# Performance work log

Hardware: AMD Instinct MI355X
Metric: run time of the kernel (lower is better)

Reference implementation:

```python
import jax, jax.numpy as jnp
import numpy as np

B, T, I, D = 16, 128, 8, 128


def layer_norm(x, g, b, eps=1e-5):
    mu = jnp.mean(x, -1, keepdims=True)
    var = jnp.mean((x - mu) ** 2, -1, keepdims=True)
    return (x - mu) * jax.lax.rsqrt(var + eps) * g + b


def setup_inputs() -> dict:
    key = jax.random.key(0)
    ks = jax.random.split(key, 8)
    vectors = jax.random.normal(ks[0], (B, T, T, I), jnp.float32)
    # structured pairwise mask: mask[b,i,j] = real[b,i] & real[b,j]
    lengths = jax.random.randint(ks[1], (B,), T // 2, T + 1)
    real = jnp.arange(T)[None, :] < lengths[:, None]  # [B,T]
    mask = real[:, :, None] & real[:, None, :]  # [B,T,T]
    s = lambda n: 1.0 / np.sqrt(n)
    W_embed = jax.random.normal(ks[2], (I, D), jnp.float32) * s(I)
    b_embed = jnp.zeros((D,), jnp.float32)
    ln1_g = jnp.ones((D,), jnp.float32)
    ln1_b = jnp.zeros((D,), jnp.float32)
    Wq = jax.random.normal(ks[3], (D, D), jnp.float32) * s(D)
    Wk = jax.random.normal(ks[4], (D, D), jnp.float32) * s(D)
    Wv = jax.random.normal(ks[5], (D, D), jnp.float32) * s(D)
    W_out = jax.random.normal(ks[6], (D, D), jnp.float32) * s(D)
    b_out = jnp.zeros((D,), jnp.float32)
    ln2_g = jnp.ones((D,), jnp.float32)
    ln2_b = jnp.zeros((D,), jnp.float32)
    return dict(vectors=vectors, mask=mask, W_embed=W_embed, b_embed=b_embed,
                ln1_g=ln1_g, ln1_b=ln1_b, Wq=Wq, Wk=Wk, Wv=Wv,
                W_out=W_out, b_out=b_out, ln2_g=ln2_g, ln2_b=ln2_b)


def reference(vectors, mask, W_embed, b_embed, ln1_g, ln1_b, Wq, Wk, Wv,
              W_out, b_out, ln2_g, ln2_b):
    Bs, Tn = vectors.shape[0], vectors.shape[1]
    Dm = W_embed.shape[1]
    square_mask = jnp.transpose(mask, (1, 2, 0))            # [T,T,B] bool
    seq = square_mask[jnp.arange(Tn), jnp.arange(Tn)]       # [T,B] bool (diagonal)
    # shared embedding stack (masked) + norm, on flattened [T*T,B,*]
    x = jnp.transpose(vectors.reshape(Bs, Tn * Tn, -1), (1, 0, 2))  # [T*T,B,I]
    mflat = square_mask.reshape(Tn * Tn, Bs, 1).astype(x.dtype)
    x = jax.nn.gelu(x @ W_embed + b_embed) * mflat
    x = layer_norm(x, ln1_g, ln1_b)
    x = x.reshape(Tn, Tn, Bs, Dm)                           # [T,T,B,D]
    keys = x @ Wk                                            # [T,T,B,D]
    values = x @ Wv                                          # [T,T,B,D]
    queries = x[jnp.arange(Tn), jnp.arange(Tn)] @ Wq         # diag gather -> [T,B,D]
    # attention mask: pairwise-real OR self
    amask = square_mask | jnp.eye(Tn, dtype=bool)[:, :, None]  # [T,T,B]
    logits = jnp.einsum('rbd,rcbd->rcb', queries, keys) / np.sqrt(Dm)
    logits = logits + jnp.where(amask, 0.0, -1e9)
    w = jax.nn.softmax(logits, axis=1)                       # [T,T,B]
    emb = jnp.einsum('rcb,rcbd->rbd', w, values)             # [T,B,D]
    # output linear block with skip connection, masked by sequence mask
    seq_f = seq[:, :, None].astype(emb.dtype)                # [T,B,1]
    h = jax.nn.gelu(emb @ W_out + b_out)
    embeddings = layer_norm(h + emb, ln2_g, ln2_b) * seq_f   # [T,B,D]
    padding_mask = ~jnp.transpose(seq)                       # [B,T]
    sequence_mask = seq[:, :, None]                          # [T,B,1]
    global_mask = jnp.ones((Tn,), dtype=bool)                # [T]
    return embeddings, padding_mask, sequence_mask, global_mask
```

## Files before the change

kernel.cpp:

```cpp
#include <hip/hip_runtime.h>
#include <hip/hip_fp16.h>
#include <math.h>

#define BB 16
#define TT 128
#define II 8
#define DD 128
#define SCALE 0.08838834764831845f

#define WS_LEN_OFF 16384


__device__ __forceinline__ float sgelu(float x) {
    float x2 = x * x;
    float w = x * (-1.5957691216f - 0.07135481627f * x2);
    float e = __expf(w);
    return __fdividef(x, 1.0f + e);
}

__device__ __forceinline__ float fast_gelu(float x) {
    float u = 1.5957691216057308f * x * (1.0f + 0.044715f * x * x);
    float e = __expf(u);
    float th = 1.0f - __fdividef(2.0f, e + 1.0f);
    return 0.5f * x * (1.0f + th);
}

__global__ void k0_compute_M(const float* __restrict__ Wq,
                             const float* __restrict__ Wk,
                             const int* __restrict__ mask,
                             float* __restrict__ M,
                             int* __restrict__ lens) {
    if (blockIdx.x == DD) {
        __shared__ int cnt[BB];
        int t = threadIdx.x;
        if (t < BB) cnt[t] = 0;
        __syncthreads();
        if (t < TT) {
            for (int b = 0; b < BB; b++) {
                if (mask[b * TT * TT + t * TT + t]) atomicAdd(&cnt[b], 1);
            }
        }
        __syncthreads();
        if (t < BB) lens[t] = cnt[t];
        return;
    }
    __shared__ float wq[DD];
    int a = blockIdx.x, e = threadIdx.x;
    wq[e] = Wq[a * DD + e];
    __syncthreads();
    const float4* wk4 = (const float4*)(Wk + e * DD);
    float acc = 0.0f;
    #pragma unroll 8
    for (int d4 = 0; d4 < DD / 4; d4++) {
        float4 w = wk4[d4];
        acc += wq[d4 * 4 + 0] * w.x + wq[d4 * 4 + 1] * w.y +
               wq[d4 * 4 + 2] * w.z + wq[d4 * 4 + 3] * w.w;
    }
    M[a * DD + e] = acc;
}

__global__ __launch_bounds__(256, 4)
void k_main(const float* __restrict__ vectors,
            const int* __restrict__ lens,
            const float* __restrict__ We,
            const float* __restrict__ be,
            const float* __restrict__ g1,
            const float* __restrict__ b1,
            const float* __restrict__ M,
            const float* __restrict__ Wv,
            const float* __restrict__ Wo,
            const float* __restrict__ bo,
            const float* __restrict__ g2,
            const float* __restrict__ b2,
            float* __restrict__ out) {
    __shared__ __half2 xsh[TT * 64];
    __shared__ float  xrs[DD];
    __shared__ float  kqs[DD];
    __shared__ float  lgt[TT];
    __shared__ float  wgt[TT];
    __shared__ float2 pbuf[256];
    __shared__ float2 sv2[64];
    __shared__ float2 emb2[64];

    int n = blockIdx.x;
    int b = n >> 7, r = n & 127;
    int t = threadIdx.x, wave = t >> 6, lane = t & 63;
    int hh = lane >> 5, sl = lane & 31;
    int dl = sl * 4;
    int len = lens[b];

    if (r >= len) {
        if (wave == 0) {
            int rb_out = r * BB + b;
            ((float2*)out)[rb_out * 64 + lane] = make_float2(0.0f, 0.0f);
            if (lane == 0) {
                out[262144 + b * TT + r] = 1.0f;
                out[264192 + r * BB + b] = 0.0f;
                if (b == 0) out[266240 + r] = 1.0f;
            }
        }
        return;
    }

    const float4* vb4 = (const float4*)(vectors + (size_t)n * TT * II);

    float4 we4[II];
    #pragma unroll
    for (int i = 0; i < II; i++) we4[i] = *(const float4*)(We + i * DD + dl);
    float4 be4 = *(const float4*)(be + dl);
    float4 g14 = *(const float4*)(g1 + dl);
    float4 b14 = *(const float4*)(b1 + dl);

    {
        float4 v0 = vb4[2 * r], v1 = vb4[2 * r + 1];
        float vv[8] = {v0.x, v0.y, v0.z, v0.w, v1.x, v1.y, v1.z, v1.w};
        float e0 = be4.x, e1 = be4.y, e2 = be4.z, e3 = be4.w;
        #pragma unroll
        for (int i = 0; i < II; i++) {
            e0 += vv[i] * we4[i].x; e1 += vv[i] * we4[i].y;
            e2 += vv[i] * we4[i].z; e3 += vv[i] * we4[i].w;
        }
        float a0 = sgelu(e0), a1 = sgelu(e1), a2 = sgelu(e2), a3 = sgelu(e3);
        float s = (a0 + a1) + (a2 + a3);
        float q = (a0 * a0 + a1 * a1) + (a2 * a2 + a3 * a3);
        #pragma unroll
        for (int o = 16; o >= 1; o >>= 1) {
            s += __shfl_xor(s, o, 64); q += __shfl_xor(q, o, 64);
        }
        float mu = s * (1.0f / 128.0f);
        float rstd = rsqrtf(q * (1.0f / 128.0f) - mu * mu + 1e-5f);
        float x0 = (a0 - mu) * rstd * g14.x + b14.x;
        float x1 = (a1 - mu) * rstd * g14.y + b14.y;
        float x2 = (a2 - mu) * rstd * g14.z + b14.z;
        float x3 = (a3 - mu) * rstd * g14.w + b14.w;
        if (t < 32) ((float4*)xrs)[sl] = make_float4(x0, x1, x2, x3);
    }
    __syncthreads();

    {
        const float2* M2 = (const float2*)M;
        float ax = 0.0f, ay = 0.0f;
        #pragma unroll 8
        for (int j = 0; j < 32; j++) {
            int a = (wave << 5) + j;
            float xv = xrs[a];
            float2 m2 = M2[a * 64 + lane];
            ax += xv * m2.x; ay += xv * m2.y;
        }
        pbuf[t] = make_float2(ax, ay);
    }
    __syncthreads();
    if (t < 64) {
        float2 p0 = pbuf[t], p1 = pbuf[64 + t], p2 = pbuf[128 + t], p3 = pbuf[192 + t];
        kqs[2 * t]     = (p0.x + p1.x + p2.x + p3.x) * SCALE;
        kqs[2 * t + 1] = (p0.y + p1.y + p2.y + p3.y) * SCALE;
    }
    __syncthreads();

    float4 kq4 = *(const float4*)&kqs[dl];
    float4 u4 = make_float4(g14.x * kq4.x, g14.y * kq4.y, g14.z * kq4.z, g14.w * kq4.w);
    float Us, C0;
    {
        float us = (u4.x + u4.y) + (u4.z + u4.w);
        float c0 = (b14.x * kq4.x + b14.y * kq4.y) + (b14.z * kq4.z + b14.w * kq4.w);
        #pragma unroll
        for (int o = 16; o >= 1; o >>= 1) {
            us += __shfl_xor(us, o, 64); c0 += __shfl_xor(c0, o, 64);
        }
        Us = us; C0 = c0;
    }

    {
        int g = (wave << 1) + hh;
        int jmax = (len - g + 15) >> 4;
        for (int j = 0; j < jmax; j++) {
            int cA = (j << 4) + g;
            int cB = cA + 8;
            float4 vA0 = vb4[2 * cA], vA1 = vb4[2 * cA + 1];
            float4 vB0 = vb4[2 * cB], vB1 = vb4[2 * cB + 1];
            float vA[8] = {vA0.x, vA0.y, vA0.z, vA0.w, vA1.x, vA1.y, vA1.z, vA1.w};
            float vB[8] = {vB0.x, vB0.y, vB0.z, vB0.w, vB1.x, vB1.y, vB1.z, vB1.w};
            float eA0 = be4.x, eA1 = be4.y, eA2 = be4.z, eA3 = be4.w;
            float eB0 = be4.x, eB1 = be4.y, eB2 = be4.z, eB3 = be4.w;
            #pragma unroll
            for (int i = 0; i < II; i++) {
                eA0 += vA[i] * we4[i].x; eA1 += vA[i] * we4[i].y;
                eA2 += vA[i] * we4[i].z; eA3 += vA[i] * we4[i].w;
                eB0 += vB[i] * we4[i].x; eB1 += vB[i] * we4[i].y;
                eB2 += vB[i] * we4[i].z; eB3 += vB[i] * we4[i].w;
            }
            float aA0 = sgelu(eA0), aA1 = sgelu(eA1), aA2 = sgelu(eA2), aA3 = sgelu(eA3);
            float aB0 = sgelu(eB0), aB1 = sgelu(eB1), aB2 = sgelu(eB2), aB3 = sgelu(eB3);
            float sA = (aA0 + aA1) + (aA2 + aA3);
            float qA = (aA0 * aA0 + aA1 * aA1) + (aA2 * aA2 + aA3 * aA3);
            float pA = (aA0 * u4.x + aA1 * u4.y) + (aA2 * u4.z + aA3 * u4.w);
            float sB = (aB0 + aB1) + (aB2 + aB3);
            float qB = (aB0 * aB0 + aB1 * aB1) + (aB2 * aB2 + aB3 * aB3);
            float pB = (aB0 * u4.x + aB1 * u4.y) + (aB2 * u4.z + aB3 * u4.w);
            #pragma unroll
            for (int o = 16; o >= 1; o >>= 1) {
                sA += __shfl_xor(sA, o, 64); qA += __shfl_xor(qA, o, 64);
                pA += __shfl_xor(pA, o, 64);
                sB += __shfl_xor(sB, o, 64); qB += __shfl_xor(qB, o, 64);
                pB += __shfl_xor(pB, o, 64);
            }
            float muA = sA * (1.0f / 128.0f), muB = sB * (1.0f / 128.0f);
            float rsA = rsqrtf(qA * (1.0f / 128.0f) - muA * muA + 1e-5f);
            float rsB = rsqrtf(qB * (1.0f / 128.0f) - muB * muB + 1e-5f);
            float xA0 = (aA0 - muA) * rsA * g14.x + b14.x;
            float xA1 = (aA1 - muA) * rsA * g14.y + b14.y;
            float xA2 = (aA2 - muA) * rsA * g14.z + b14.z;
            float xA3 = (aA3 - muA) * rsA * g14.w + b14.w;
            float xB0 = (aB0 - muB) * rsB * g14.x + b14.x;
            float xB1 = (aB1 - muB) * rsB * g14.y + b14.y;
            float xB2 = (aB2 - muB) * rsB * g14.z + b14.z;
            float xB3 = (aB3 - muB) * rsB * g14.w + b14.w;
            {
                __half2 p0 = __floats2half2_rn(xA0, xA1), p1 = __floats2half2_rn(xA2, xA3);
                uint2 st; st.x = *(unsigned*)&p0; st.y = *(unsigned*)&p1;
                ((uint2*)(xsh + cA * 64))[sl] = st;
                if (sl == 0) lgt[cA] = rsA * (pA - muA * Us) + C0;
            }
            if (cB < len) {
                __half2 p0 = __floats2half2_rn(xB0, xB1), p1 = __floats2half2_rn(xB2, xB3);
                uint2 st; st.x = *(unsigned*)&p0; st.y = *(unsigned*)&p1;
                ((uint2*)(xsh + cB * 64))[sl] = st;
                if (sl == 0) lgt[cB] = rsB * (pB - muB * Us) + C0;
            }
        }
    }
    __syncthreads();

    if (wave == 0) {
        float l0 = lgt[lane];
        float l1 = (lane + 64 < len) ? lgt[lane + 64] : -1e9f;
        float mx = fmaxf(l0, l1);
        #pragma unroll
        for (int o = 32; o >= 1; o >>= 1) mx = fmaxf(mx, __shfl_xor(mx, o, 64));
        float e0 = __expf(l0 - mx), e1 = __expf(l1 - mx);
        float s = e0 + e1;
        #pragma unroll
        for (int o = 32; o >= 1; o >>= 1) s += __shfl_xor(s, o, 64);
        float inv = __fdividef(1.0f, s);
        wgt[lane] = e0 * inv; wgt[lane + 64] = e1 * inv;
    }
    __syncthreads();

    {
        int jw = (len - wave + 3) >> 2;
        float ax = 0.0f, ay = 0.0f;
        for (int j = 0; j < jw; j++) {
            int c = (j << 2) + wave;
            float w = wgt[c];
            float2 xf = __half22float2(xsh[c * 64 + lane]);
            ax += w * xf.x; ay += w * xf.y;
        }
        pbuf[t] = make_float2(ax, ay);
    }
    __syncthreads();
    if (t < 64) {
        float2 p0 = pbuf[t], p1 = pbuf[64 + t], p2 = pbuf[128 + t], p3 = pbuf[192 + t];
        sv2[t] = make_float2(p0.x + p1.x + p2.x + p3.x, p0.y + p1.y + p2.y + p3.y);
    }
    __syncthreads();

    {
        const float* svf = (const float*)sv2;
        const float2* Wv2 = (const float2*)Wv;
        float ax = 0.0f, ay = 0.0f;
        #pragma unroll 8
        for (int j = 0; j < 32; j++) {
            int a = (wave << 5) + j;
            float s = svf[a];
            float2 w2 = Wv2[a * 64 + lane];
            ax += s * w2.x; ay += s * w2.y;
        }
        pbuf[t] = make_float2(ax, ay);
    }
    __syncthreads();
    if (t < 64) {
        float2 p0 = pbuf[t], p1 = pbuf[64 + t], p2 = pbuf[128 + t], p3 = pbuf[192 + t];
        emb2[t] = make_float2(p0.x + p1.x + p2.x + p3.x, p0.y + p1.y + p2.y + p3.y);
    }
    __syncthreads();

    {
        const float* ef = (const float*)emb2;
        const float2* Wo2 = (const float2*)Wo;
        float ax = 0.0f, ay = 0.0f;
        #pragma unroll 8
        for (int j = 0; j < 32; j++) {
            int a = (wave << 5) + j;
            float s = ef[a];
            float2 w2 = Wo2[a * 64 + lane];
            ax += s * w2.x; ay += s * w2.y;
        }
        pbuf[t] = make_float2(ax, ay);
    }
    __syncthreads();

    if (wave == 0) {
        float2 p0 = pbuf[lane], p1 = pbuf[64 + lane], p2 = pbuf[128 + lane], p3 = pbuf[192 + lane];
        float2 bo2 = ((const float2*)bo)[lane];
        float2 em = emb2[lane];
        float h0 = fast_gelu(p0.x + p1.x + p2.x + p3.x + bo2.x);
        float h1 = fast_gelu(p0.y + p1.y + p2.y + p3.y + bo2.y);
        float z0 = h0 + em.x, z1 = h1 + em.y;
        float s = z0 + z1, q = z0 * z0 + z1 * z1;
        #pragma unroll
        for (int o = 32; o >= 1; o >>= 1) {
            s += __shfl_xor(s, o, 64); q += __shfl_xor(q, o, 64);
        }
        float mu = s * (1.0f / 128.0f);
        float rstd = rsqrtf(q * (1.0f / 128.0f) - mu * mu + 1e-5f);
        float2 g22 = ((const float2*)g2)[lane], b22 = ((const float2*)b2)[lane];
        float u0 = z0 - mu, u1 = z1 - mu;
        int rb_out = r * BB + b;
        ((float2*)out)[rb_out * 64 + lane] =
            make_float2(u0 * rstd * g22.x + b22.x,
                        u1 * rstd * g22.y + b22.y);
        if (lane == 0) {
            out[262144 + b * TT + r] = 0.0f;
            out[264192 + r * BB + b] = 1.0f;
            if (b == 0) out[266240 + r] = 1.0f;
        }
    }
}

extern "C" void kernel_launch(void* const* d_in, const int* in_sizes, int n_in,
                              void* d_out, int out_size, void* d_ws, size_t ws_size,
                              hipStream_t stream) {
    const float* vectors = (const float*)d_in[0];
    const int*   mask    = (const int*)d_in[1];
    const float* W_embed = (const float*)d_in[2];
    const float* b_embed = (const float*)d_in[3];
    const float* ln1_g   = (const float*)d_in[4];
    const float* ln1_b   = (const float*)d_in[5];
    const float* Wq      = (const float*)d_in[6];
    const float* Wk      = (const float*)d_in[7];
    const float* Wv      = (const float*)d_in[8];
    const float* W_out   = (const float*)d_in[9];
    const float* b_out   = (const float*)d_in[10];
    const float* ln2_g   = (const float*)d_in[11];
    const float* ln2_b   = (const float*)d_in[12];
    float* out = (float*)d_out;

    float* M    = (float*)d_ws;
    int*   lens = (int*)((float*)d_ws + WS_LEN_OFF);

    hipLaunchKernelGGL(k0_compute_M, dim3(DD + 1), dim3(DD), 0, stream,
                       Wq, Wk, mask, M, lens);
    hipLaunchKernelGGL(k_main, dim3(TT * BB), dim3(256), 0, stream,
                       vectors, lens, W_embed, b_embed, ln1_g, ln1_b, M,
                       Wv, W_out, b_out, ln2_g, ln2_b, out);
}
```

Measured before the change: 136.6 us.

## Precompute Wv·Wout product and compute logits from shared fp16 rows after the embed loop

Adds a setup pass that precomputes Wv@Wout, so the main kernel gets emb and the pre-activation h from one matvec split across waves instead of two dependent matvecs with an extra barrier. The separate diagonal-row embedding and the early query projection are removed. The query row is taken from the main embed loop, and logits are recomputed as dot products over the fp16 shared-memory rows. This trades the in-loop fused logit reductions for a later pass over the fp16 tile, which adds rounding error to the logits and a few more barriers.

```diff
diff --git a/kernel.cpp b/kernel.cpp
--- a/kernel.cpp
+++ b/kernel.cpp
@@ -8,7 +8,8 @@
 #define DD 128
 #define SCALE 0.08838834764831845f
 
-#define WS_LEN_OFF 16384
+#define WS_WVO_OFF 16384
+#define WS_LEN_OFF 32768
 
 
 __device__ __forceinline__ float sgelu(float x) {
@@ -25,38 +26,51 @@
     return 0.5f * x * (1.0f + th);
 }
 
-__global__ void k0_compute_M(const float* __restrict__ Wq,
-                             const float* __restrict__ Wk,
-                             const int* __restrict__ mask,
-                             float* __restrict__ M,
-                             int* __restrict__ lens) {
-    if (blockIdx.x == DD) {
+__global__ void k0_setup(const float* __restrict__ Wq,
+                         const float* __restrict__ Wk,
+                         const float* __restrict__ Wv,
+                         const float* __restrict__ Wo,
+                         const int* __restrict__ mask,
+                         float* __restrict__ M,
+                         float* __restrict__ WvWo,
+                         int* __restrict__ lens) {
+    int blk = blockIdx.x;
+    if (blk == DD) {
         __shared__ int cnt[BB];
         int t = threadIdx.x;
         if (t < BB) cnt[t] = 0;
         __syncthreads();
-        if (t < TT) {
-            for (int b = 0; b < BB; b++) {
-                if (mask[b * TT * TT + t * TT + t]) atomicAdd(&cnt[b], 1);
-            }
+        for (int b = 0; b < BB; b++) {
+            if (mask[b * TT * TT + t * TT + t]) atomicAdd(&cnt[b], 1);
         }
         __syncthreads();
         if (t < BB) lens[t] = cnt[t];
         return;
     }
-    __shared__ float wq[DD];
-    int a = blockIdx.x, e = threadIdx.x;
-    wq[e] = Wq[a * DD + e];
-    __syncthreads();
-    const float4* wk4 = (const float4*)(Wk + e * DD);
-    float acc = 0.0f;
-    #pragma unroll 8
-    for (int d4 = 0; d4 < DD / 4; d4++) {
-        float4 w = wk4[d4];
-        acc += wq[d4 * 4 + 0] * w.x + wq[d4 * 4 + 1] * w.y +
-               wq[d4 * 4 + 2] * w.z + wq[d4 * 4 + 3] * w.w;
-    }
-    M[a * DD + e] = acc;
+    __shared__ float row[DD];
+    int d = threadIdx.x;
+    if (blk < DD) {
+        int a = blk;
+        row[d] = Wq[a * DD + d];
+        __syncthreads();
+        const float4* wk4 = (const float4*)(Wk + d * DD);
+        float acc = 0.0f;
+        #pragma unroll 8
+        for (int e4 = 0; e4 < DD / 4; e4++) {
+            float4 w = wk4[e4];
+            acc += row[e4 * 4 + 0] * w.x + row[e4 * 4 + 1] * w.y +
+                   row[e4 * 4 + 2] * w.z + row[e4 * 4 + 3] * w.w;
+        }
+        M[a * DD + d] = acc;
+    } else {
+        int a = blk - DD - 1;
+        row[d] = Wv[a * DD + d];
+        __syncthreads();
+        float acc = 0.0f;
+        #pragma unroll 8
+        for (int e = 0; e < DD; e++) acc += row[e] * Wo[e * DD + d];
+        WvWo[a * DD + d] = acc;
+    }
 }
 
 __global__ __launch_bounds__(256, 4)
@@ -68,7 +82,7 @@
             const float* __restrict__ b1,
             const float* __restrict__ M,
             const float* __restrict__ Wv,
-            const float* __restrict__ Wo,
+            const float* __restrict__ WvWo,
             const float* __restrict__ bo,
             const float* __restrict__ g2,
             const float* __restrict__ b2,
@@ -80,7 +94,6 @@
     __shared__ float  wgt[TT];
     __shared__ float2 pbuf[256];
     __shared__ float2 sv2[64];
-    __shared__ float2 emb2[64];
 
     int n = blockIdx.x;
     int b = n >> 7, r = n & 127;
@@ -110,65 +123,6 @@
     float4 be4 = *(const float4*)(be + dl);
     float4 g14 = *(const float4*)(g1 + dl);
     float4 b14 = *(const float4*)(b1 + dl);
-
-    {
-        float4 v0 = vb4[2 * r], v1 = vb4[2 * r + 1];
-        float vv[8] = {v0.x, v0.y, v0.z, v0.w, v1.x, v1.y, v1.z, v1.w};
-        float e0 = be4.x, e1 = be4.y, e2 = be4.z, e3 = be4.w;
-        #pragma unroll
-        for (int i = 0; i < II; i++) {
-            e0 += vv[i] * we4[i].x; e1 += vv[i] * we4[i].y;
-            e2 += vv[i] * we4[i].z; e3 += vv[i] * we4[i].w;
-        }
-        float a0 = sgelu(e0), a1 = sgelu(e1), a2 = sgelu(e2), a3 = sgelu(e3);
-        float s = (a0 + a1) + (a2 + a3);
-        float q = (a0 * a0 + a1 * a1) + (a2 * a2 + a3 * a3);
-        #pragma unroll
-        for (int o = 16; o >= 1; o >>= 1) {
-            s += __shfl_xor(s, o, 64); q += __shfl_xor(q, o, 64);
-        }
-        float mu = s * (1.0f / 128.0f);
-        float rstd = rsqrtf(q * (1.0f / 128.0f) - mu * mu + 1e-5f);
-        float x0 = (a0 - mu) * rstd * g14.x + b14.x;
-        float x1 = (a1 - mu) * rstd * g14.y + b14.y;
-        float x2 = (a2 - mu) * rstd * g14.z + b14.z;
-        float x3 = (a3 - mu) * rstd * g14.w + b14.w;
-        if (t < 32) ((float4*)xrs)[sl] = make_float4(x0, x1, x2, x3);
-    }
-    __syncthreads();
-
-    {
-        const float2* M2 = (const float2*)M;
-        float ax = 0.0f, ay = 0.0f;
-        #pragma unroll 8
-        for (int j = 0; j < 32; j++) {
-            int a = (wave << 5) + j;
-            float xv = xrs[a];
-            float2 m2 = M2[a * 64 + lane];
-            ax += xv * m2.x; ay += xv * m2.y;
-        }
-        pbuf[t] = make_float2(ax, ay);
-    }
-    __syncthreads();
-    if (t < 64) {
-        float2 p0 = pbuf[t], p1 = pbuf[64 + t], p2 = pbuf[128 + t], p3 = pbuf[192 + t];
-        kqs[2 * t]     = (p0.x + p1.x + p2.x + p3.x) * SCALE;
-        kqs[2 * t + 1] = (p0.y + p1.y + p2.y + p3.y) * SCALE;
-    }
-    __syncthreads();
-
-    float4 kq4 = *(const float4*)&kqs[dl];
-    float4 u4 = make_float4(g14.x * kq4.x, g14.y * kq4.y, g14.z * kq4.z, g14.w * kq4.w);
-    float Us, C0;
-    {
-        float us = (u4.x + u4.y) + (u4.z + u4.w);
-        float c0 = (b14.x * kq4.x + b14.y * kq4.y) + (b14.z * kq4.z + b14.w * kq4.w);
-        #pragma unroll
-        for (int o = 16; o >= 1; o >>= 1) {
-            us += __shfl_xor(us, o, 64); c0 += __shfl_xor(c0, o, 64);
-        }
-        Us = us; C0 = c0;
-    }
 
     {
         int g = (wave << 1) + hh;
@@ -193,16 +147,12 @@
             float aB0 = sgelu(eB0), aB1 = sgelu(eB1), aB2 = sgelu(eB2), aB3 = sgelu(eB3);
             float sA = (aA0 + aA1) + (aA2 + aA3);
             float qA = (aA0 * aA0 + aA1 * aA1) + (aA2 * aA2 + aA3 * aA3);
-            float pA = (aA0 * u4.x + aA1 * u4.y) + (aA2 * u4.z + aA3 * u4.w);
             float sB = (aB0 + aB1) + (aB2 + aB3);
             float qB = (aB0 * aB0 + aB1 * aB1) + (aB2 * aB2 + aB3 * aB3);
-            float pB = (aB0 * u4.x + aB1 * u4.y) + (aB2 * u4.z + aB3 * u4.w);
             #pragma unroll
             for (int o = 16; o >= 1; o >>= 1) {
                 sA += __shfl_xor(sA, o, 64); qA += __shfl_xor(qA, o, 64);
-                pA += __shfl_xor(pA, o, 64);
                 sB += __shfl_xor(sB, o, 64); qB += __shfl_xor(qB, o, 64);
-                pB += __shfl_xor(pB, o, 64);
             }
             float muA = sA * (1.0f / 128.0f), muB = sB * (1.0f / 128.0f);
             float rsA = rsqrtf(qA * (1.0f / 128.0f) - muA * muA + 1e-5f);
@@ -219,14 +169,52 @@
                 __half2 p0 = __floats2half2_rn(xA0, xA1), p1 = __floats2half2_rn(xA2, xA3);
                 uint2 st; st.x = *(unsigned*)&p0; st.y = *(unsigned*)&p1;
                 ((uint2*)(xsh + cA * 64))[sl] = st;
-                if (sl == 0) lgt[cA] = rsA * (pA - muA * Us) + C0;
+                if (cA == r) ((float4*)xrs)[sl] = make_float4(xA0, xA1, xA2, xA3);
             }
             if (cB < len) {
                 __half2 p0 = __floats2half2_rn(xB0, xB1), p1 = __floats2half2_rn(xB2, xB3);
                 uint2 st; st.x = *(unsigned*)&p0; st.y = *(unsigned*)&p1;
                 ((uint2*)(xsh + cB * 64))[sl] = st;
-                if (sl == 0) lgt[cB] = rsB * (pB - muB * Us) + C0;
-            }
+                if (cB == r) ((float4*)xrs)[sl] = make_float4(xB0, xB1, xB2, xB3);
+            }
+        }
+    }
+    __syncthreads();
+
+    {
+        const float2* M2 = (const float2*)M;
+        float ax = 0.0f, ay = 0.0f;
+        #pragma unroll 8
+        for (int j = 0; j < 32; j++) {
+            int a = (wave << 5) + j;
+            float xv = xrs[a];
+            float2 m2 = M2[a * 64 + lane];
+            ax += xv * m2.x; ay += xv * m2.y;
+        }
+        pbuf[t] = make_float2(ax, ay);
+    }
+    __syncthreads();
+    if (t < 64) {
+        float2 p0 = pbuf[t], p1 = pbuf[64 + t], p2 = pbuf[128 + t], p3 = pbuf[192 + t];
+        kqs[2 * t]     = (p0.x + p1.x + p2.x + p3.x) * SCALE;
+        kqs[2 * t + 1] = (p0.y + p1.y + p2.y + p3.y) * SCALE;
+    }
+    __syncthreads();
+
+    {
+        int c = t >> 1, p = t & 1;
+        if (c < len) {
+            const float2* kq2 = (const float2*)kqs;
+            float acc = 0.0f;
+            #pragma unroll 8
+            for (int j = 0; j < 32; j++) {
+                int idx = (p << 5) + ((j + c) & 31);
+                float2 xf = __half22float2(xsh[c * 64 + idx]);
+                float2 kv = kq2[idx];
+                acc += xf.x * kv.x + xf.y * kv.y;
+            }
+            acc += __shfl_xor(acc, 1, 64);
+            if (p == 0) lgt[c] = acc;
         }
     }
     __syncthreads();
@@ -266,46 +254,28 @@
 
     {
         const float* svf = (const float*)sv2;
-        const float2* Wv2 = (const float2*)Wv;
+        const float2* W2 = (wave < 2) ? (const float2*)Wv : (const float2*)WvWo;
+        int abase = (wave & 1) << 6;
         float ax = 0.0f, ay = 0.0f;
         #pragma unroll 8
-        for (int j = 0; j < 32; j++) {
-            int a = (wave << 5) + j;
+        for (int j = 0; j < 64; j++) {
+            int a = abase + j;
             float s = svf[a];
-            float2 w2 = Wv2[a * 64 + lane];
+            float2 w2 = W2[a * 64 + lane];
             ax += s * w2.x; ay += s * w2.y;
         }
         pbuf[t] = make_float2(ax, ay);
     }
     __syncthreads();
-    if (t < 64) {
-        float2 p0 = pbuf[t], p1 = pbuf[64 + t], p2 = pbuf[128 + t], p3 = pbuf[192 + t];
-        emb2[t] = make_float2(p0.x + p1.x + p2.x + p3.x, p0.y + p1.y + p2.y + p3.y);
-    }
-    __syncthreads();
-
-    {
-        const float* ef = (const float*)emb2;
-        const float2* Wo2 = (const float2*)Wo;
-        float ax = 0.0f, ay = 0.0f;
-        #pragma unroll 8
-        for (int j = 0; j < 32; j++) {
-            int a = (wave << 5) + j;
-            float s = ef[a];
-            float2 w2 = Wo2[a * 64 + lane];
-            ax += s * w2.x; ay += s * w2.y;
-        }
-        pbuf[t] = make_float2(ax, ay);
-    }
-    __syncthreads();
 
     if (wave == 0) {
-        float2 p0 = pbuf[lane], p1 = pbuf[64 + lane], p2 = pbuf[128 + lane], p3 = pbuf[192 + lane];
+        float2 e0 = pbuf[lane], e1 = pbuf[64 + lane];
+        float2 h0p = pbuf[128 + lane], h1p = pbuf[192 + lane];
         float2 bo2 = ((const float2*)bo)[lane];
-        float2 em = emb2[lane];
-        float h0 = fast_gelu(p0.x + p1.x + p2.x + p3.x + bo2.x);
-        float h1 = fast_gelu(p0.y + p1.y + p2.y + p3.y + bo2.y);
-        float z0 = h0 + em.x, z1 = h1 + em.y;
+        float em0 = e0.x + e1.x, em1 = e0.y + e1.y;
+        float h0 = fast_gelu(h0p.x + h1p.x + bo2.x);
+        float h1 = fast_gelu(h0p.y + h1p.y + bo2.y);
+        float z0 = h0 + em0, z1 = h1 + em1;
         float s = z0 + z1, q = z0 * z0 + z1 * z1;
         #pragma unroll
         for (int o = 32; o >= 1; o >>= 1) {
@@ -346,11 +316,12 @@
     float* out = (float*)d_out;
 
     float* M    = (float*)d_ws;
+    float* WvWo = (float*)d_ws + WS_WVO_OFF;
     int*   lens = (int*)((float*)d_ws + WS_LEN_OFF);
 
-    hipLaunchKernelGGL(k0_compute_M, dim3(DD + 1), dim3(DD), 0, stream,
-                       Wq, Wk, mask, M, lens);
+    hipLaunchKernelGGL(k0_setup, dim3(2 * DD + 1), dim3(DD), 0, stream,
+                       Wq, Wk, Wv, W_out, mask, M, WvWo, lens);
     hipLaunchKernelGGL(k_main, dim3(TT * BB), dim3(256), 0, stream,
                        vectors, lens, W_embed, b_embed, ln1_g, ln1_b, M,
-                       Wv, W_out, b_out, ln2_g, ln2_b, out);
-}
+                       Wv, WvWo, b_out, ln2_g, ln2_b, out);
+}
```

New measurement: 136.7 us. No clear change (+0.1%).
